# Kernel tuning notes

Hardware: AMD Instinct MI355X
Metric: run time of the kernel (lower is better)

## Reference

```python
import jax, jax.numpy as jnp
import numpy as np

VOX = 64      # vox_size
KS = 21       # smooth_ks (odd -> 'SAME' == pad ks//2)
SIGMA = 3.0   # smooth_sigma


def smoothing_kernel():
    # normalized 1D gaussian used separably along the 3 voxel axes
    x = jnp.arange(KS, dtype=jnp.float32) - (KS - 1) / 2.0
    g = jnp.exp(-(x * x) / (2.0 * SIGMA * SIGMA))
    return g / g.sum()


def pc_voxels(pc, size):
    """Trilinear scatter of points in [-0.5,0.5]^3 into a [B,size,size,size] grid."""
    B, N, _ = pc.shape
    g = (pc + 0.5) * (size - 1)            # grid coords
    fl = jnp.floor(g)
    idx = fl.astype(jnp.int32)             # [B,N,3] lower corner
    frac = g - fl                          # trilinear fractions
    # 8 corner offsets in {0,1}^3
    offs = jnp.array([[(i >> 2) & 1, (i >> 1) & 1, i & 1] for i in range(8)], dtype=jnp.int32)
    pos = idx[:, :, None, :] + offs[None, None]                       # [B,N,8,3]
    w = jnp.prod(jnp.where(offs[None, None].astype(bool),
                           frac[:, :, None, :], 1.0 - frac[:, :, None, :]), axis=-1)  # [B,N,8]
    inb = jnp.all((pos >= 0) & (pos < size), axis=-1)
    w = jnp.where(inb, w, 0.0)
    posc = jnp.clip(pos, 0, size - 1)
    # voxel layout vox[b, z, y, x]; pc columns are (x, y, z)
    flat = posc[..., 2] * (size * size) + posc[..., 1] * size + posc[..., 0]
    vox = jnp.zeros((B, size * size * size), pc.dtype)
    vox = vox.at[jnp.arange(B)[:, None, None], flat].add(w)
    return jnp.clip(vox.reshape(B, size, size, size), 0.0, 1.0)


def voxels_smooth(v, g1d, scale):
    """Separable 3D Gaussian smoothing + per-batch scale, clamped to [0,1]."""
    x = v[:, None]  # NCDHW, C=1
    ks = g1d.shape[0]
    for kshape in ((1, 1, ks, 1, 1), (1, 1, 1, ks, 1), (1, 1, 1, 1, ks)):
        x = jax.lax.conv_general_dilated(
            x, g1d.reshape(kshape), (1, 1, 1), 'SAME',
            dimension_numbers=('NCDHW', 'OIDHW', 'NCDHW'))
    x = x[:, 0] * scale[:, None, None, None]
    return jnp.clip(x, 0.0, 1.0)


def drc_prob(v):
    """DRC ray-termination probabilities along depth (axis 1)."""
    trans = jnp.cumprod(1.0 - v, axis=1)                                   # [B,D,H,W]
    tshift = jnp.concatenate([jnp.ones_like(trans[:, :1]), trans[:, :-1]], axis=1)
    stop = v * tshift                                                      # stop at voxel d
    esc = trans[:, -1:]                                                    # ray escapes
    return jnp.concatenate([stop, esc], axis=1)                            # [B,D+1,H,W]


def reference(pc, rotation, scale):
    pc_t = jnp.einsum('bni,bji->bnj', pc, rotation)   # camera transform: pc @ R^T
    vox = pc_voxels(pc_t, VOX)
    sm = voxels_smooth(vox, smoothing_kernel(), scale)
    prob = drc_prob(sm)
    proj = prob[:, :-1].sum(1)[:, ::-1, :]            # sum over depth, flip rows
    return proj


def setup_inputs() -> dict:
    key = jax.random.key(0)
    k1, k2, k3 = jax.random.split(key, 3)
    B, N = 32, 65536
    pc = jax.random.uniform(k1, (B, N, 3), jnp.float32) - 0.5   # points in [-0.5, 0.5]
    q, _ = jnp.linalg.qr(jax.random.normal(k2, (B, 3, 3), jnp.float32))  # random rotations
    scale = 0.5 + jax.random.uniform(k3, (B,), jnp.float32)
    return {"pc": pc, "rotation": q, "scale": scale}
```

## Files before the change

### kernel.cpp

```cpp
#include <hip/hip_runtime.h>

#define NB    32
#define NP    65536
#define SZ    64
#define SZ3   (SZ * SZ * SZ)
#define KS    21
#define HALF  10
#define NBIN  65
#define CAP   2048
#define FXS   960.0f

typedef _Float16 half8_t __attribute__((ext_vector_type(8)));
typedef _Float16 half4_t __attribute__((ext_vector_type(4)));
typedef float    f32x4_t __attribute__((ext_vector_type(4)));

__device__ __forceinline__ int swz(int row, int col) {
    return (row << 6) + ((((col >> 3) ^ (row & 7))) << 3) + (col & 7);
}

__device__ __forceinline__ void weights_reg(float* w) {
    float sum = 0.0f;
#pragma unroll
    for (int k = 0; k < KS; ++k) {
        float d = (float)k - (float)HALF;
        w[k] = expf(-d * d / 18.0f);
        sum += w[k];
    }
#pragma unroll
    for (int k = 0; k < KS; ++k) w[k] /= sum;
}

__device__ __forceinline__ void fma4(float4& a, float t, const float4& v) {
    a.x = fmaf(t, v.x, a.x); a.y = fmaf(t, v.y, a.y);
    a.z = fmaf(t, v.z, a.z); a.w = fmaf(t, v.w, a.w);
}

__device__ __forceinline__ unsigned pack_fx(float g) {
    float c = fminf(fmaxf(g, -2.0f), 65.0f);
    return (unsigned)__float2uint_rn((c + 2.0f) * FXS);
}

__global__ void fill_kernel(const float* __restrict__ pc,
                            const float* __restrict__ rot,
                            int* __restrict__ cur,
                            uint2* __restrict__ binned,
                            _Float16* __restrict__ Gg) {
    __shared__ int lcnt[NBIN];
    __shared__ int lbase[NBIN];
    int base = blockIdx.x * 1024;
    int b = base >> 16;
    if (threadIdx.x < NBIN) lcnt[threadIdx.x] = 0;
    __syncthreads();
    const float* R = rot + b * 9;
    const float4* p4 = (const float4*)(pc + (size_t)base * 3);
    float4 f0 = p4[threadIdx.x * 3 + 0];
    float4 f1 = p4[threadIdx.x * 3 + 1];
    float4 f2 = p4[threadIdx.x * 3 + 2];
    float px[4] = {f0.x, f0.w, f1.z, f2.y};
    float py[4] = {f0.y, f1.x, f1.w, f2.z};
    float pz[4] = {f0.z, f1.y, f2.x, f2.w};
    uint2 pk[4];
    int bin[4], lpos[4];
#pragma unroll
    for (int j = 0; j < 4; ++j) {
        float g0 = (R[0] * px[j] + R[1] * py[j] + R[2] * pz[j] + 0.5f) * 63.0f;
        float g1 = (R[3] * px[j] + R[4] * py[j] + R[5] * pz[j] + 0.5f) * 63.0f;
        float g2 = (R[6] * px[j] + R[7] * py[j] + R[8] * pz[j] + 0.5f) * 63.0f;
        int i2 = (int)floorf(g2);
        bin[j] = (i2 >= -1 && i2 <= 63) ? i2 + 1 : -1;
        pk[j] = make_uint2(pack_fx(g0) | (pack_fx(g1) << 16), pack_fx(g2));
        if (bin[j] >= 0) lpos[j] = atomicAdd(&lcnt[bin[j]], 1);
    }
    __syncthreads();
    if (threadIdx.x < NBIN) {
        int c = lcnt[threadIdx.x];
        lbase[threadIdx.x] = c ? atomicAdd(&cur[b * NBIN + threadIdx.x], c) : 0;
    }
    __syncthreads();
#pragma unroll
    for (int j = 0; j < 4; ++j)
        if (bin[j] >= 0) {
            int pos = lbase[bin[j]] + lpos[j];
            if (pos < CAP)
                binned[(size_t)(b * NBIN + bin[j]) * CAP + pos] = pk[j];
        }
    if (blockIdx.x == 0) {
        float w[KS];
        weights_reg(w);
        for (int i = threadIdx.x; i < 4096; i += 256) {
            int d = (i >> 6) - (i & 63) + HALF;
            Gg[i] = ((unsigned)d < (unsigned)KS) ? (_Float16)w[d] : (_Float16)0.0f;
        }
    }
}

__global__ void __launch_bounds__(64) splat_blur(const uint2* __restrict__ binned,
                                                 const int* __restrict__ cur,
                                                 const _Float16* __restrict__ Gg,
                                                 _Float16* __restrict__ vox) {
    __shared__ __align__(16) _Float16 Ay[65 * 64];
    __shared__ __align__(16) _Float16 Bx[65 * 64];
    int lane = threadIdx.x;
    int b = blockIdx.x >> 6, z = blockIdx.x & 63;
    int q = lane >> 4, c = lane & 15;

    {
        int4 z4 = {0, 0, 0, 0};
        int4* a4 = (int4*)Ay;
        int4* b4 = (int4*)Bx;
        for (int i = lane; i < 65 * 64 * 2 / 16; i += 64) { a4[i] = z4; b4[i] = z4; }
    }

    half8_t gf[4][2];
#pragma unroll
    for (int ni = 0; ni < 4; ++ni)
#pragma unroll
        for (int h = 0; h < 2; ++h)
            gf[ni][h] = *(const half8_t*)&Gg[(ni * 16 + c) * 64 + h * 32 + q * 8];

    int c0 = min(cur[b * NBIN + z],     CAP);
    int c1 = min(cur[b * NBIN + z + 1], CAP);
    const uint2* s0 = binned + (size_t)(b * NBIN + z) * CAP;
    const uint2* s1 = binned + (size_t)(b * NBIN + z + 1) * CAP;
    int n = c0 + c1;

    f32x4_t acc[4][4];
#pragma unroll
    for (int mi = 0; mi < 4; ++mi)
#pragma unroll
        for (int ni = 0; ni < 4; ++ni) acc[mi][ni] = (f32x4_t){0.f, 0.f, 0.f, 0.f};

    int iters = (n + 63) >> 6;
    uint2 nxt = make_uint2(0u, 0u);
    if (lane < n) nxt = (lane < c0) ? s0[lane] : s1[lane - c0];
    for (int it = 0; it < iters; ++it) {
        uint2 pk = nxt;
        int ni2 = (it + 1) * 64 + lane;
        nxt = make_uint2(0u, 0u);
        if (ni2 < n) nxt = (ni2 < c0) ? s0[ni2] : s1[ni2 - c0];

        float gx = (float)(pk.x & 0xffffu) * (1.0f / FXS) - 2.0f;
        float gy = (float)(pk.x >> 16)     * (1.0f / FXS) - 2.0f;
        float gz = (float)(pk.y & 0xffffu) * (1.0f / FXS) - 2.0f;
        float f0 = floorf(gx), f1 = floorf(gy);
        int   i0 = (int)f0,    i1 = (int)f1;
        float r0 = gx - f0,    r1f = gy - f1;
        float az = fmaxf(0.0f, 1.0f - fabsf(gz - (float)z));
        int ylo = ((unsigned)i1       < 64u) ? i1       : 64;
        int yhi = ((unsigned)(i1 + 1) < 64u) ? (i1 + 1) : 64;
        int xlo = ((unsigned)i0       < 64u) ? i0       : 64;
        int xhi = ((unsigned)(i0 + 1) < 64u) ? (i0 + 1) : 64;
        Ay[swz(ylo, lane)] = (_Float16)(az * (1.0f - r1f));
        Ay[swz(yhi, lane)] = (_Float16)(az * r1f);
        Bx[swz(xlo, lane)] = (_Float16)(1.0f - r0);
        Bx[swz(xhi, lane)] = (_Float16)r0;
#pragma unroll
        for (int h = 0; h < 2; ++h) {
            half8_t af[4], bf[4];
#pragma unroll
            for (int mi = 0; mi < 4; ++mi)
                af[mi] = *(const half8_t*)&Ay[swz(mi * 16 + c, h * 32 + q * 8)];
#pragma unroll
            for (int ni = 0; ni < 4; ++ni)
                bf[ni] = *(const half8_t*)&Bx[swz(ni * 16 + c, h * 32 + q * 8)];
#pragma unroll
            for (int mi = 0; mi < 4; ++mi)
#pragma unroll
                for (int ni = 0; ni < 4; ++ni)
                    acc[mi][ni] = __builtin_amdgcn_mfma_f32_16x16x32_f16(
                        af[mi], bf[ni], acc[mi][ni], 0, 0, 0);
        }
        Ay[swz(ylo, lane)] = (_Float16)0.0f;
        Ay[swz(yhi, lane)] = (_Float16)0.0f;
        Bx[swz(xlo, lane)] = (_Float16)0.0f;
        Bx[swz(xhi, lane)] = (_Float16)0.0f;
    }

    asm volatile("" ::: "memory");
    _Float16* P = Ay;
    _Float16* T = Bx;

#pragma unroll
    for (int mi = 0; mi < 4; ++mi)
#pragma unroll
        for (int ni = 0; ni < 4; ++ni)
#pragma unroll
            for (int r = 0; r < 4; ++r)
                P[swz(mi * 16 + q * 4 + r, ni * 16 + c)] =
                    (_Float16)fminf(fmaxf(acc[mi][ni][r], 0.0f), 1.0f);
    asm volatile("" ::: "memory");

    f32x4_t a2[4][4];
#pragma unroll
    for (int mi = 0; mi < 4; ++mi)
#pragma unroll
        for (int ni = 0; ni < 4; ++ni) a2[mi][ni] = (f32x4_t){0.f, 0.f, 0.f, 0.f};
#pragma unroll
    for (int h = 0; h < 2; ++h) {
        half8_t af[4];
#pragma unroll
        for (int mi = 0; mi < 4; ++mi)
            af[mi] = *(const half8_t*)&P[swz(mi * 16 + c, h * 32 + q * 8)];
#pragma unroll
        for (int mi = 0; mi < 4; ++mi)
#pragma unroll
            for (int ni = 0; ni < 4; ++ni)
                a2[mi][ni] = __builtin_amdgcn_mfma_f32_16x16x32_f16(
                    af[mi], gf[ni][h], a2[mi][ni], 0, 0, 0);
    }
    asm volatile("" ::: "memory");

#pragma unroll
    for (int mi = 0; mi < 4; ++mi)
#pragma unroll
        for (int ni = 0; ni < 4; ++ni) {
            half4_t pkd;
#pragma unroll
            for (int r = 0; r < 4; ++r) pkd[r] = (_Float16)a2[mi][ni][r];
            *(half4_t*)&T[swz(ni * 16 + c, mi * 16 + q * 4)] = pkd;
        }
    asm volatile("" ::: "memory");

    f32x4_t a3[4][4];
#pragma unroll
    for (int mi = 0; mi < 4; ++mi)
#pragma unroll
        for (int ni = 0; ni < 4; ++ni) a3[mi][ni] = (f32x4_t){0.f, 0.f, 0.f, 0.f};
#pragma unroll
    for (int h = 0; h < 2; ++h) {
        half8_t bf[4];
#pragma unroll
        for (int ni = 0; ni < 4; ++ni)
            bf[ni] = *(const half8_t*)&T[swz(ni * 16 + c, h * 32 + q * 8)];
#pragma unroll
        for (int mi = 0; mi < 4; ++mi)
#pragma unroll
            for (int ni = 0; ni < 4; ++ni)
                a3[mi][ni] = __builtin_amdgcn_mfma_f32_16x16x32_f16(
                    gf[mi][h], bf[ni], a3[mi][ni], 0, 0, 0);
    }

    _Float16* dst = vox + ((size_t)b << 18) + ((size_t)z << 12);
#pragma unroll
    for (int mi = 0; mi < 4; ++mi)
#pragma unroll
        for (int ni = 0; ni < 4; ++ni)
#pragma unroll
            for (int r = 0; r < 4; ++r)
                dst[((mi * 16 + q * 4 + r) << 6) + ni * 16 + c] = (_Float16)a3[mi][ni][r];
}

__global__ void convz_drc_kernel(const _Float16* __restrict__ in,
                                 const float* __restrict__ scale,
                                 float* __restrict__ out) {
    __shared__ float sraw[640 + SZ * SZ + 640];
    __shared__ float c[SZ * SZ];
    __shared__ float segS[4][64], segT[4][64];
    float* s = sraw + 640;
    int b = blockIdx.x >> 6, y = blockIdx.x & 63;

    for (int i = threadIdx.x; i < 640; i += 256) {
        sraw[i] = 0.0f;
        sraw[640 + SZ * SZ + i] = 0.0f;
    }
    const _Float16* base = in + ((size_t)b << 18) + (y << 6);
#pragma unroll
    for (int g = 0; g < 4; ++g) {
        int cell = g * 256 + threadIdx.x;
        int z = cell >> 4, xc = (cell & 15) << 2;
        half4_t v = *(const half4_t*)&base[((size_t)z << 12) + xc];
        float4 f = make_float4((float)v[0], (float)v[1], (float)v[2], (float)v[3]);
        *(float4*)&s[(z << 6) + xc] = f;
    }
    __syncthreads();

    float w[KS];
    weights_reg(w);

    {
        int z0 = (threadIdx.x >> 4) << 2;
        int xc = (threadIdx.x & 15) << 2;
        float4 a0 = {0,0,0,0}, a1 = {0,0,0,0}, a2 = {0,0,0,0}, a3 = {0,0,0,0};
#pragma unroll
        for (int d = 0; d < 24; ++d) {
            int zz = z0 - HALF + d;
            float4 v = *(const float4*)&s[(zz << 6) + xc];
            if (d <= 20)           fma4(a0, w[d],     v);
            if (d >= 1 && d <= 21) fma4(a1, w[d - 1], v);
            if (d >= 2 && d <= 22) fma4(a2, w[d - 2], v);
            if (d >= 3)            fma4(a3, w[d - 3], v);
        }
        *(float4*)&c[((z0 + 0) << 6) + xc] = a0;
        *(float4*)&c[((z0 + 1) << 6) + xc] = a1;
        *(float4*)&c[((z0 + 2) << 6) + xc] = a2;
        *(float4*)&c[((z0 + 3) << 6) + xc] = a3;
    }
    __syncthreads();

    {
        int x = threadIdx.x & 63, seg = threadIdx.x >> 6;
        float sc = scale[b];
        float trans = 1.0f, sum = 0.0f;
#pragma unroll
        for (int zz = 0; zz < 16; ++zz) {
            int z = seg * 16 + zz;
            float v = fminf(fmaxf(c[(z << 6) + x] * sc, 0.0f), 1.0f);
            sum += v * trans;
            trans *= 1.0f - v;
        }
        segS[seg][x] = sum;
        segT[seg][x] = trans;
    }
    __syncthreads();
    if (threadIdx.x < 64) {
        int x = threadIdx.x;
        float t = 1.0f, S = 0.0f;
#pragma unroll
        for (int sgi = 0; sgi < 4; ++sgi) { S += segS[sgi][x] * t; t *= segT[sgi][x]; }
        out[(b << 12) + ((63 - y) << 6) + x] = S;
    }
}

extern "C" void kernel_launch(void* const* d_in, const int* in_sizes, int n_in,
                              void* d_out, int out_size, void* d_ws, size_t ws_size,
                              hipStream_t stream) {
    const float* pc    = (const float*)d_in[0];
    const float* rot   = (const float*)d_in[1];
    const float* scale = (const float*)d_in[2];
    float* out = (float*)d_out;

    _Float16* vox    = (_Float16*)d_ws;
    uint2*    binned = (uint2*)((char*)d_ws + (size_t)NB * SZ3 * sizeof(_Float16));
    _Float16* Gg     = (_Float16*)((char*)binned + (size_t)NB * NBIN * CAP * sizeof(uint2));
    int*      cur    = (int*)((char*)Gg + 64 * 64 * sizeof(_Float16));

    hipMemsetAsync(cur, 0, NB * NBIN * sizeof(int), stream);

    fill_kernel     <<<NB * NP / 1024, 256, 0, stream>>>(pc, rot, cur, binned, Gg);
    splat_blur      <<<NB * SZ, 64, 0, stream>>>(binned, cur, Gg, vox);
    convz_drc_kernel<<<NB * SZ, 256, 0, stream>>>(vox, scale, out);
}
```

Measured before the change: 126.6 us.

## Split splat point loop across two waves and use per-wave bin histograms

The splat_blur kernel now runs two wavefronts per block. Each wave processes alternate 64-point chunks into its own LDS tiles and accumulates its own MFMA results. Wave 1 then writes its accumulators through LDS so wave 0 can add them before the blur stages, and wave 1 exits. The fill kernel also switches to per-wave shared histograms with prefix offsets to cut LDS atomic contention. The cost is doubled LDS per block, an extra reduction and a barrier, and an idle wave during the later blur stages.

```diff
diff --git a/kernel.cpp b/kernel.cpp
--- a/kernel.cpp
+++ b/kernel.cpp
@@ -45,11 +45,13 @@
                             int* __restrict__ cur,
                             uint2* __restrict__ binned,
                             _Float16* __restrict__ Gg) {
-    __shared__ int lcnt[NBIN];
+    __shared__ int h[4][NBIN];
+    __shared__ int woff[4][NBIN];
     __shared__ int lbase[NBIN];
     int base = blockIdx.x * 1024;
     int b = base >> 16;
-    if (threadIdx.x < NBIN) lcnt[threadIdx.x] = 0;
+    int wv = threadIdx.x >> 6;
+    for (int i = threadIdx.x; i < 4 * NBIN; i += 256) h[i / NBIN][i % NBIN] = 0;
     __syncthreads();
     const float* R = rot + b * 9;
     const float4* p4 = (const float4*)(pc + (size_t)base * 3);
@@ -69,18 +71,21 @@
         int i2 = (int)floorf(g2);
         bin[j] = (i2 >= -1 && i2 <= 63) ? i2 + 1 : -1;
         pk[j] = make_uint2(pack_fx(g0) | (pack_fx(g1) << 16), pack_fx(g2));
-        if (bin[j] >= 0) lpos[j] = atomicAdd(&lcnt[bin[j]], 1);
+        if (bin[j] >= 0) lpos[j] = atomicAdd(&h[wv][bin[j]], 1);
     }
     __syncthreads();
     if (threadIdx.x < NBIN) {
-        int c = lcnt[threadIdx.x];
-        lbase[threadIdx.x] = c ? atomicAdd(&cur[b * NBIN + threadIdx.x], c) : 0;
+        int t = threadIdx.x;
+        int s0 = h[0][t], s1 = h[1][t], s2 = h[2][t], s3 = h[3][t];
+        int tot = s0 + s1 + s2 + s3;
+        lbase[t] = tot ? atomicAdd(&cur[b * NBIN + t], tot) : 0;
+        woff[0][t] = 0; woff[1][t] = s0; woff[2][t] = s0 + s1; woff[3][t] = s0 + s1 + s2;
     }
     __syncthreads();
 #pragma unroll
     for (int j = 0; j < 4; ++j)
         if (bin[j] >= 0) {
-            int pos = lbase[bin[j]] + lpos[j];
+            int pos = lbase[bin[j]] + woff[wv][bin[j]] + lpos[j];
             if (pos < CAP)
                 binned[(size_t)(b * NBIN + bin[j]) * CAP + pos] = pk[j];
         }
@@ -94,29 +99,32 @@
     }
 }
 
-__global__ void __launch_bounds__(64) splat_blur(const uint2* __restrict__ binned,
-                                                 const int* __restrict__ cur,
-                                                 const _Float16* __restrict__ Gg,
-                                                 _Float16* __restrict__ vox) {
-    __shared__ __align__(16) _Float16 Ay[65 * 64];
-    __shared__ __align__(16) _Float16 Bx[65 * 64];
-    int lane = threadIdx.x;
+__global__ void __launch_bounds__(128) splat_blur(const uint2* __restrict__ binned,
+                                                  const int* __restrict__ cur,
+                                                  const _Float16* __restrict__ Gg,
+                                                  _Float16* __restrict__ vox) {
+    __shared__ __align__(16) _Float16 tiles[2][2][65 * 64];
+    int tid = threadIdx.x;
+    int wv = tid >> 6, lane = tid & 63;
     int b = blockIdx.x >> 6, z = blockIdx.x & 63;
     int q = lane >> 4, c = lane & 15;
+    _Float16* Ay = tiles[wv][0];
+    _Float16* Bx = tiles[wv][1];
 
     {
         int4 z4 = {0, 0, 0, 0};
-        int4* a4 = (int4*)Ay;
-        int4* b4 = (int4*)Bx;
-        for (int i = lane; i < 65 * 64 * 2 / 16; i += 64) { a4[i] = z4; b4[i] = z4; }
+        int4* a4 = (int4*)tiles[wv];
+        for (int i = lane; i < 2 * 65 * 64 * 2 / 16; i += 64) a4[i] = z4;
     }
 
     half8_t gf[4][2];
-#pragma unroll
-    for (int ni = 0; ni < 4; ++ni)
-#pragma unroll
-        for (int h = 0; h < 2; ++h)
-            gf[ni][h] = *(const half8_t*)&Gg[(ni * 16 + c) * 64 + h * 32 + q * 8];
+    if (wv == 0) {
+#pragma unroll
+        for (int ni = 0; ni < 4; ++ni)
+#pragma unroll
+            for (int h = 0; h < 2; ++h)
+                gf[ni][h] = *(const half8_t*)&Gg[(ni * 16 + c) * 64 + h * 32 + q * 8];
+    }
 
     int c0 = min(cur[b * NBIN + z],     CAP);
     int c1 = min(cur[b * NBIN + z + 1], CAP);
@@ -132,10 +140,13 @@
 
     int iters = (n + 63) >> 6;
     uint2 nxt = make_uint2(0u, 0u);
-    if (lane < n) nxt = (lane < c0) ? s0[lane] : s1[lane - c0];
-    for (int it = 0; it < iters; ++it) {
+    {
+        int i0g = wv * 64 + lane;
+        if (i0g < n) nxt = (i0g < c0) ? s0[i0g] : s1[i0g - c0];
+    }
+    for (int it = wv; it < iters; it += 2) {
         uint2 pk = nxt;
-        int ni2 = (it + 1) * 64 + lane;
+        int ni2 = (it + 2) * 64 + lane;
         nxt = make_uint2(0u, 0u);
         if (ni2 < n) nxt = (ni2 < c0) ? s0[ni2] : s1[ni2 - c0];
 
@@ -177,9 +188,29 @@
     }
 
     asm volatile("" ::: "memory");
+    float* Cst = (float*)tiles[1];
+    if (wv == 1) {
+#pragma unroll
+        for (int mi = 0; mi < 4; ++mi)
+#pragma unroll
+            for (int ni = 0; ni < 4; ++ni)
+#pragma unroll
+                for (int r = 0; r < 4; ++r)
+                    Cst[(mi * 16 + q * 4 + r) * 65 + ni * 16 + c] = acc[mi][ni][r];
+    }
+    __syncthreads();
+    if (wv == 1) return;
+
+#pragma unroll
+    for (int mi = 0; mi < 4; ++mi)
+#pragma unroll
+        for (int ni = 0; ni < 4; ++ni)
+#pragma unroll
+            for (int r = 0; r < 4; ++r)
+                acc[mi][ni][r] += Cst[(mi * 16 + q * 4 + r) * 65 + ni * 16 + c];
+
     _Float16* P = Ay;
     _Float16* T = Bx;
-
 #pragma unroll
     for (int mi = 0; mi < 4; ++mi)
 #pragma unroll
@@ -337,6 +368,6 @@
     hipMemsetAsync(cur, 0, NB * NBIN * sizeof(int), stream);
 
     fill_kernel     <<<NB * NP / 1024, 256, 0, stream>>>(pc, rot, cur, binned, Gg);
-    splat_blur      <<<NB * SZ, 64, 0, stream>>>(binned, cur, Gg, vox);
+    splat_blur      <<<NB * SZ, 128, 0, stream>>>(binned, cur, Gg, vox);
     convz_drc_kernel<<<NB * SZ, 256, 0, stream>>>(vox, scale, out);
 }
```

New measurement: 136.1 us. +7.5%, slower.
